# Performance work log

Hardware: AMD Instinct MI355X
Metric: run time of the kernel (lower is better)

Reference implementation:

```python
import jax, jax.numpy as jnp
import numpy as np

U, I, D, L, NNZ, B = 100000, 50000, 64, 3, 3200000, 4096
N = U + I
MOMENTUM = 0.05

def setup_inputs() -> dict:
    key = jax.random.key(0)
    ks = jax.random.split(key, 10)
    return {
        'user_emb': jax.random.normal(ks[0], (U, D), jnp.float32) * 0.02,
        'item_emb': jax.random.normal(ks[1], (I, D), jnp.float32) * 0.02,
        'W': jax.random.normal(ks[2], (D, D), jnp.float32) * (1.0 / np.sqrt(D)),
        'b': jnp.zeros((D,), jnp.float32),
        'adj_rows': jax.random.randint(ks[3], (NNZ,), 0, N, jnp.int32),
        'adj_cols': jax.random.randint(ks[4], (NNZ,), 0, N, jnp.int32),
        'adj_vals': jax.random.uniform(ks[5], (NNZ,), jnp.float32) * 0.05,
        'users': jax.random.randint(ks[6], (B,), 0, U, jnp.int32),
        'items': jax.random.randint(ks[7], (B,), 0, I, jnp.int32),
        'u_his': jax.random.normal(ks[8], (U, D), jnp.float32),
        'i_his': jax.random.normal(ks[9], (I, D), jnp.float32),
    }

def _spmm(rows, cols, vals, x):
    # y = A @ x for sparse COO A: gather source rows, scale, scatter-add to dest rows
    return jax.ops.segment_sum(vals[:, None] * x[cols], rows, num_segments=N)

def reference(user_emb, item_emb, W, b, adj_rows, adj_cols, adj_vals, users, items, u_his, i_his):
    ego = jnp.concatenate([user_emb, item_emb], axis=0)  # [N, D]
    acc = ego
    cur = ego
    for _ in range(L):
        cur = _spmm(adj_rows, adj_cols, adj_vals, cur)
        acc = acc + cur
    all_emb = acc / (L + 1)           # mean over stacked layers
    u_all = all_emb[:U]
    i_all = all_emb[U:]
    u_online = u_all[users]           # [B, D]
    i_online = i_all[items]
    m = MOMENTUM
    u_target = jax.lax.stop_gradient(u_his[users] * m + u_online * (1.0 - m))
    i_target = jax.lax.stop_gradient(i_his[items] * m + i_online * (1.0 - m))
    p_u = u_online @ W.T + b
    p_i = i_online @ W.T + b
    return (p_u, u_target, p_i, i_target)
```

## Files before the change

### kernel.cpp

```cpp
#include <hip/hip_runtime.h>
#include <hip/hip_bf16.h>

#define U_CNT   100000
#define I_CNT   50000
#define D_DIM   64
#define N_NODES 150000
#define NNZ_E   3200000
#define B_SZ    4096

#define NSUB 1172
#define CAP2 4096
#define TILE_E 8192
#define N_TILES ((NNZ_E + TILE_E - 1) / TILE_E)

#define CONV_THREADS (N_NODES * 16)
#define CONV_PER_BLK (512 * 4)
#define CONV_BLOCKS ((CONV_THREADS + CONV_PER_BLK - 1) / CONV_PER_BLK)

typedef unsigned int uint;
typedef unsigned short ushort_t;
typedef _Float16 half_t;
typedef half_t half2_t __attribute__((ext_vector_type(2)));

union h2u_t { uint u; half2_t h; };
__device__ __forceinline__ half2_t u2h2(uint u) { h2u_t c; c.u = u; return c.h; }
__device__ __forceinline__ uint h22u(half2_t h) { h2u_t c; c.h = h; return c.u; }
__device__ __forceinline__ half2_t h2shfl_xor(half2_t v, int m) {
    h2u_t c; c.h = v; c.u = (uint)__shfl_xor((int)c.u, m, 64); return c.h;
}
__device__ __forceinline__ float h2lo(uint u) { return (float)u2h2(u)[0]; }
__device__ __forceinline__ float h2hi(uint u) { return (float)u2h2(u)[1]; }

__global__ __launch_bounds__(256) void init_cursors_kernel(int* __restrict__ subcursor) {
    int i = blockIdx.x * 256 + threadIdx.x;
    if (i < NSUB) subcursor[i] = i * CAP2;
}

__global__ __launch_bounds__(512) void scatter_kernel(const int* __restrict__ rows,
                                                      const int* __restrict__ cols,
                                                      const float* __restrict__ vals,
                                                      int* __restrict__ subcursor,
                                                      int2* __restrict__ meta,
                                                      const float4* __restrict__ ue4,
                                                      const float4* __restrict__ ie4,
                                                      uint2* __restrict__ e2) {
    int tid = threadIdx.x;

    if (blockIdx.x >= N_TILES) {
        int g0 = (blockIdx.x - N_TILES) * CONV_PER_BLK + tid;
        #pragma unroll
        for (int k = 0; k < 4; ++k) {
            int g = g0 + k * 512;
            if (g < CONV_THREADS) {
                float4 f = (g < U_CNT * 16) ? ue4[g] : ie4[g - U_CNT * 16];
                half2_t a = { (half_t)f.x, (half_t)f.y };
                half2_t b = { (half_t)f.z, (half_t)f.w };
                uint2 o; o.x = h22u(a); o.y = h22u(b);
                e2[g] = o;
            }
        }
        return;
    }

    __shared__ int lcnt[NSUB];
    __shared__ int gbase[NSUB];

    for (int i = tid; i < NSUB; i += 512) lcnt[i] = 0;
    __syncthreads();

    int base = blockIdx.x * TILE_E;
    int nk = NNZ_E - base - tid;
    nk = (nk <= 0) ? 0 : (nk + 511) >> 9;

    int pk[16]; float vv[16]; int sb[16]; int rk[16];
    #pragma unroll
    for (int k = 0; k < 16; ++k) {
        if (k < nk) {
            int j = base + tid + (k << 9);
            int r = rows[j];
            int c = cols[j];
            vv[k] = vals[j];
            sb[k] = r >> 7;
            pk[k] = ((r & 127) << 18) | c;
            rk[k] = atomicAdd(&lcnt[sb[k]], 1);
        }
    }
    __syncthreads();

    for (int i = tid; i < NSUB; i += 512) {
        int c = lcnt[i];
        gbase[i] = (c > 0) ? atomicAdd(&subcursor[i], c) : 0;
    }
    __syncthreads();

    #pragma unroll
    for (int k = 0; k < 16; ++k) {
        if (k < nk) {
            int pos = gbase[sb[k]] + rk[k];
            if (pos < (sb[k] + 1) * CAP2)
                meta[pos] = make_int2(pk[k], __float_as_int(vv[k]));
        }
    }
}

__global__ __launch_bounds__(256) void row_sort_kernel(const int* __restrict__ subcursor,
                                                       int2* __restrict__ meta,
                                                       int* __restrict__ rstart,
                                                       int* __restrict__ rend) {
    __shared__ int2 stage[CAP2];
    __shared__ int rcnt[128];
    __shared__ int scan[128];
    __shared__ int cur[128];
    int g = blockIdx.x;
    int base = g * CAP2;
    int cnt = subcursor[g] - base;
    if (cnt > CAP2) cnt = CAP2;
    int tid = threadIdx.x;
    int r0 = g << 7;

    if (tid < 128) rcnt[tid] = 0;
    __syncthreads();

    for (int i = tid; i < cnt; i += 256) {
        int2 e = meta[base + i];
        stage[i] = e;
        atomicAdd(&rcnt[((uint)e.x >> 18) & 127], 1);
    }
    __syncthreads();

    if (tid < 128) scan[tid] = rcnt[tid];
    __syncthreads();
    for (int off = 1; off < 128; off <<= 1) {
        int t = (tid < 128 && tid >= off) ? scan[tid - off] : 0;
        __syncthreads();
        if (tid < 128) scan[tid] += t;
        __syncthreads();
    }
    if (tid < 128) {
        int excl = scan[tid] - rcnt[tid];
        cur[tid] = excl;
        int r = r0 + tid;
        if (r < N_NODES) {
            rstart[r] = base + excl;
            rend[r]   = base + scan[tid];
        }
    }
    __syncthreads();

    for (int i = tid; i < cnt; i += 256) {
        int2 e = stage[i];
        int rl = ((uint)e.x >> 18) & 127;
        int pos = atomicAdd(&cur[rl], 1);
        float v = __int_as_float(e.y);
        half2_t hv = { (half_t)v, (half_t)v };
        meta[base + pos] = make_int2(e.x & 0x3FFFF, (int)h22u(hv));
    }
}

__global__ __launch_bounds__(256) void spmm_fp16_kernel(const int* __restrict__ rstart,
                                                        const int* __restrict__ rend,
                                                        const int2* __restrict__ csr,
                                                        const ushort_t* __restrict__ x,
                                                        ushort_t* __restrict__ out) {
    int wid  = (blockIdx.x * blockDim.x + threadIdx.x) >> 6;
    int lane = threadIdx.x & 63;
    int sub  = lane >> 3;
    int l8   = lane & 7;
    if (wid >= N_NODES) return;
    int s = rstart[wid], e = rend[wid];
    const uint4* x4 = (const uint4*)x;

    int last = e - 1; if (last < s) last = s;
    auto ld = [&](int jj) -> int2 {
        int2 c = csr[jj < e ? jj : last];
        if (jj >= e) c.y = 0;
        return c;
    };

    half2_t a0 = { (half_t)0, (half_t)0 };
    half2_t a1 = a0, a2 = a0, a3 = a0;

    int j = s + sub;
    int2 c0 = ld(j);
    int2 c1 = ld(j + 8);
    int2 c2 = ld(j + 16);
    int2 c3 = ld(j + 24);
    for (; j < e; j += 32) {
        uint4 x0 = x4[(size_t)(c0.x & 0x3FFFF) * 8 + l8];
        uint4 x1 = x4[(size_t)(c1.x & 0x3FFFF) * 8 + l8];
        uint4 x2 = x4[(size_t)(c2.x & 0x3FFFF) * 8 + l8];
        uint4 x3 = x4[(size_t)(c3.x & 0x3FFFF) * 8 + l8];
        int jn = j + 32;
        int2 n0 = ld(jn);
        int2 n1 = ld(jn + 8);
        int2 n2 = ld(jn + 16);
        int2 n3 = ld(jn + 24);
        half2_t v0 = u2h2((uint)c0.y);
        a0 += u2h2(x0.x) * v0; a1 += u2h2(x0.y) * v0;
        a2 += u2h2(x0.z) * v0; a3 += u2h2(x0.w) * v0;
        half2_t v1 = u2h2((uint)c1.y);
        a0 += u2h2(x1.x) * v1; a1 += u2h2(x1.y) * v1;
        a2 += u2h2(x1.z) * v1; a3 += u2h2(x1.w) * v1;
        half2_t v2 = u2h2((uint)c2.y);
        a0 += u2h2(x2.x) * v2; a1 += u2h2(x2.y) * v2;
        a2 += u2h2(x2.z) * v2; a3 += u2h2(x2.w) * v2;
        half2_t v3 = u2h2((uint)c3.y);
        a0 += u2h2(x3.x) * v3; a1 += u2h2(x3.y) * v3;
        a2 += u2h2(x3.z) * v3; a3 += u2h2(x3.w) * v3;
        c0 = n0; c1 = n1; c2 = n2; c3 = n3;
    }
    a0 += h2shfl_xor(a0, 8);  a1 += h2shfl_xor(a1, 8);
    a2 += h2shfl_xor(a2, 8);  a3 += h2shfl_xor(a3, 8);
    a0 += h2shfl_xor(a0, 16); a1 += h2shfl_xor(a1, 16);
    a2 += h2shfl_xor(a2, 16); a3 += h2shfl_xor(a3, 16);
    a0 += h2shfl_xor(a0, 32); a1 += h2shfl_xor(a1, 32);
    a2 += h2shfl_xor(a2, 32); a3 += h2shfl_xor(a3, 32);

    if (sub == 0) {
        uint4 r;
        r.x = h22u(a0); r.y = h22u(a1); r.z = h22u(a2); r.w = h22u(a3);
        ((uint4*)out)[(size_t)wid * 8 + l8] = r;
    }
}

__global__ __launch_bounds__(256) void epilogue_kernel(const int* __restrict__ users,
                                                       const int* __restrict__ items,
                                                       const int* __restrict__ rstart,
                                                       const int* __restrict__ rend,
                                                       const int2* __restrict__ csr,
                                                       const ushort_t* __restrict__ ebuf,
                                                       const ushort_t* __restrict__ buf1,
                                                       const ushort_t* __restrict__ buf2,
                                                       const float* __restrict__ u_his,
                                                       const float* __restrict__ i_his,
                                                       const float* __restrict__ W,
                                                       const float* __restrict__ bvec,
                                                       float* __restrict__ out) {
    __shared__ float Wt[D_DIM * 65];
    __shared__ float bsh[D_DIM];
    __shared__ float on_s[4][D_DIM];
    for (int t = threadIdx.x; t < D_DIM * D_DIM; t += blockDim.x) {
        int j = t >> 6, k = t & 63;
        Wt[k * 65 + j] = W[t];
    }
    if (threadIdx.x < D_DIM) bsh[threadIdx.x] = bvec[threadIdx.x];

    int wv   = threadIdx.x >> 6;
    int wid  = blockIdx.x * 4 + wv;
    int lane = threadIdx.x & 63;
    int sub  = lane >> 4;
    int l16  = lane & 15;

    bool is_user = (wid < B_SZ);
    int  samp = is_user ? wid : wid - B_SZ;
    int  idx  = is_user ? users[samp] : items[samp];
    int  row  = is_user ? idx : (U_CNT + idx);

    const float* his = is_user ? u_his : i_his;
    float hisv = his[(size_t)idx * D_DIM + lane];
    uint2 eg = make_uint2(0, 0), b1v = eg, b2v = eg;
    if (sub == 0) {
        eg  = ((const uint2*)ebuf)[(size_t)row * 16 + l16];
        b1v = ((const uint2*)buf1)[(size_t)row * 16 + l16];
        b2v = ((const uint2*)buf2)[(size_t)row * 16 + l16];
    }

    int s = rstart[row], e = rend[row];
    int last = e - 1; if (last < s) last = s;
    auto ld = [&](int jj) -> int2 {
        int2 c = csr[jj < e ? jj : last];
        if (jj >= e) c.y = 0;
        return c;
    };
    half2_t c0 = { (half_t)0, (half_t)0 };
    half2_t c1 = c0;
    int j = s + sub;
    int2 e0 = ld(j);
    int2 e1 = ld(j + 4);
    int2 e2 = ld(j + 8);
    int2 e3 = ld(j + 12);
    for (; j < e; j += 16) {
        uint2 x0 = ((const uint2*)buf2)[(size_t)(e0.x & 0x3FFFF) * 16 + l16];
        uint2 x1 = ((const uint2*)buf2)[(size_t)(e1.x & 0x3FFFF) * 16 + l16];
        uint2 x2 = ((const uint2*)buf2)[(size_t)(e2.x & 0x3FFFF) * 16 + l16];
        uint2 x3 = ((const uint2*)buf2)[(size_t)(e3.x & 0x3FFFF) * 16 + l16];
        int jn = j + 16;
        int2 n0 = ld(jn);
        int2 n1 = ld(jn + 4);
        int2 n2 = ld(jn + 8);
        int2 n3 = ld(jn + 12);
        half2_t v0 = u2h2((uint)e0.y);
        c0 += u2h2(x0.x) * v0; c1 += u2h2(x0.y) * v0;
        half2_t v1 = u2h2((uint)e1.y);
        c0 += u2h2(x1.x) * v1; c1 += u2h2(x1.y) * v1;
        half2_t v2 = u2h2((uint)e2.y);
        c0 += u2h2(x2.x) * v2; c1 += u2h2(x2.y) * v2;
        half2_t v3 = u2h2((uint)e3.y);
        c0 += u2h2(x3.x) * v3; c1 += u2h2(x3.y) * v3;
        e0 = n0; e1 = n1; e2 = n2; e3 = n3;
    }
    c0 += h2shfl_xor(c0, 16); c1 += h2shfl_xor(c1, 16);
    c0 += h2shfl_xor(c0, 32); c1 += h2shfl_xor(c1, 32);

    if (sub == 0) {
        on_s[wv][l16 * 4 + 0] = (h2lo(eg.x) + h2lo(b1v.x) + h2lo(b2v.x) + (float)c0[0]) * 0.25f;
        on_s[wv][l16 * 4 + 1] = (h2hi(eg.x) + h2hi(b1v.x) + h2hi(b2v.x) + (float)c0[1]) * 0.25f;
        on_s[wv][l16 * 4 + 2] = (h2lo(eg.y) + h2lo(b1v.y) + h2lo(b2v.y) + (float)c1[0]) * 0.25f;
        on_s[wv][l16 * 4 + 3] = (h2hi(eg.y) + h2hi(b1v.y) + h2hi(b2v.y) + (float)c1[1]) * 0.25f;
    }
    __syncthreads();

    float online = on_s[wv][lane];
    float target = 0.05f * hisv + 0.95f * online;

    float p = bsh[lane];
    #pragma unroll
    for (int k = 0; k < D_DIM; ++k) {
        float ok = __shfl(online, k, 64);
        p = fmaf(ok, Wt[k * 65 + lane], p);
    }

    size_t base = is_user ? 0 : (size_t)2 * B_SZ * D_DIM;
    out[base + (size_t)samp * D_DIM + lane] = p;
    out[base + (size_t)B_SZ * D_DIM + (size_t)samp * D_DIM + lane] = target;
}


extern "C" void kernel_launch(void* const* d_in, const int* in_sizes, int n_in,
                              void* d_out, int out_size, void* d_ws, size_t ws_size,
                              hipStream_t stream) {
    const float* user_emb = (const float*)d_in[0];
    const float* item_emb = (const float*)d_in[1];
    const float* W        = (const float*)d_in[2];
    const float* bvec     = (const float*)d_in[3];
    const int*   adj_rows = (const int*)d_in[4];
    const int*   adj_cols = (const int*)d_in[5];
    const float* adj_vals = (const float*)d_in[6];
    const int*   users    = (const int*)d_in[7];
    const int*   items    = (const int*)d_in[8];
    const float* u_his    = (const float*)d_in[9];
    const float* i_his    = (const float*)d_in[10];
    float* out = (float*)d_out;

    char* ws = (char*)d_ws;
    size_t o = 0;
    ushort_t* ebuf  = (ushort_t*)(ws + o); o += (size_t)N_NODES * D_DIM * 2;
    ushort_t* buf1  = (ushort_t*)(ws + o); o += (size_t)N_NODES * D_DIM * 2;
    ushort_t* buf2  = (ushort_t*)(ws + o); o += (size_t)N_NODES * D_DIM * 2;
    int2*  meta     = (int2*)(ws + o);     o += (size_t)NSUB * CAP2 * 8;
    int*   rstart   = (int*)(ws + o);      o += (size_t)N_NODES * 4;
    int*   rend     = (int*)(ws + o);      o += (size_t)N_NODES * 4;
    int*   subcursor= (int*)(ws + o);      o += (size_t)NSUB * 4;
    (void)ws_size; (void)o; (void)in_sizes; (void)n_in; (void)out_size;

    init_cursors_kernel<<<(NSUB + 255) / 256, 256, 0, stream>>>(subcursor);
    scatter_kernel<<<N_TILES + CONV_BLOCKS, 512, 0, stream>>>(
        adj_rows, adj_cols, adj_vals, subcursor, meta,
        (const float4*)user_emb, (const float4*)item_emb, (uint2*)ebuf);
    row_sort_kernel<<<NSUB, 256, 0, stream>>>(subcursor, meta, rstart, rend);

    int spmm_blocks = (N_NODES + 3) / 4;
    spmm_fp16_kernel<<<spmm_blocks, 256, 0, stream>>>(rstart, rend, meta, ebuf, buf1);
    spmm_fp16_kernel<<<spmm_blocks, 256, 0, stream>>>(rstart, rend, meta, buf1, buf2);

    epilogue_kernel<<<(2 * B_SZ) / 4, 256, 0, stream>>>(users, items, rstart, rend, meta,
                                                        ebuf, buf1, buf2,
                                                        u_his, i_his, W, bvec, out);
}
```

Baseline: 335.0 us.

## Use larger two-pass scatter tiles and a wavefront-shuffle row scan

The COO scatter kernel now runs 256-thread blocks over 16K-edge tiles in two passes. The first pass only counts rows per sub-bucket, and the second re-reads rows, cols and vals and places each edge. This halves the number of global cursor atomics and per-block LDS initialisations, and frees the registers that held 16 staged edges. The cost is reading the row indices twice. The row_sort prefix sum over 128 rows is replaced by a single-wavefront shuffle scan over pairs, which removes the shared scan array and many barriers.

```diff
diff --git a/kernel.cpp b/kernel.cpp
--- a/kernel.cpp
+++ b/kernel.cpp
@@ -10,11 +10,11 @@
 
 #define NSUB 1172
 #define CAP2 4096
-#define TILE_E 8192
+#define TILE_E 16384
 #define N_TILES ((NNZ_E + TILE_E - 1) / TILE_E)
 
 #define CONV_THREADS (N_NODES * 16)
-#define CONV_PER_BLK (512 * 4)
+#define CONV_PER_BLK (256 * 4)
 #define CONV_BLOCKS ((CONV_THREADS + CONV_PER_BLK - 1) / CONV_PER_BLK)
 
 typedef unsigned int uint;
@@ -36,7 +36,7 @@
     if (i < NSUB) subcursor[i] = i * CAP2;
 }
 
-__global__ __launch_bounds__(512) void scatter_kernel(const int* __restrict__ rows,
+__global__ __launch_bounds__(256) void scatter_kernel(const int* __restrict__ rows,
                                                       const int* __restrict__ cols,
                                                       const float* __restrict__ vals,
                                                       int* __restrict__ subcursor,
@@ -50,7 +50,7 @@
         int g0 = (blockIdx.x - N_TILES) * CONV_PER_BLK + tid;
         #pragma unroll
         for (int k = 0; k < 4; ++k) {
-            int g = g0 + k * 512;
+            int g = g0 + k * 256;
             if (g < CONV_THREADS) {
                 float4 f = (g < U_CNT * 16) ? ue4[g] : ie4[g - U_CNT * 16];
                 half2_t a = { (half_t)f.x, (half_t)f.y };
@@ -65,40 +65,42 @@
     __shared__ int lcnt[NSUB];
     __shared__ int gbase[NSUB];
 
-    for (int i = tid; i < NSUB; i += 512) lcnt[i] = 0;
+    for (int i = tid; i < NSUB; i += 256) lcnt[i] = 0;
     __syncthreads();
 
     int base = blockIdx.x * TILE_E;
-    int nk = NNZ_E - base - tid;
-    nk = (nk <= 0) ? 0 : (nk + 511) >> 9;
-
-    int pk[16]; float vv[16]; int sb[16]; int rk[16];
-    #pragma unroll
-    for (int k = 0; k < 16; ++k) {
-        if (k < nk) {
-            int j = base + tid + (k << 9);
-            int r = rows[j];
-            int c = cols[j];
-            vv[k] = vals[j];
-            sb[k] = r >> 7;
-            pk[k] = ((r & 127) << 18) | c;
-            rk[k] = atomicAdd(&lcnt[sb[k]], 1);
+    int end = base + TILE_E; if (end > NNZ_E) end = NNZ_E;
+
+    for (int j0 = base; j0 < end; j0 += 4096) {
+        #pragma unroll
+        for (int k = 0; k < 16; ++k) {
+            int j = j0 + tid + (k << 8);
+            if (j < end) atomicAdd(&lcnt[rows[j] >> 7], 1);
         }
     }
     __syncthreads();
 
-    for (int i = tid; i < NSUB; i += 512) {
+    for (int i = tid; i < NSUB; i += 256) {
         int c = lcnt[i];
         gbase[i] = (c > 0) ? atomicAdd(&subcursor[i], c) : 0;
-    }
-    __syncthreads();
-
-    #pragma unroll
-    for (int k = 0; k < 16; ++k) {
-        if (k < nk) {
-            int pos = gbase[sb[k]] + rk[k];
-            if (pos < (sb[k] + 1) * CAP2)
-                meta[pos] = make_int2(pk[k], __float_as_int(vv[k]));
+        lcnt[i] = 0;
+    }
+    __syncthreads();
+
+    for (int j0 = base; j0 < end; j0 += 4096) {
+        #pragma unroll
+        for (int k = 0; k < 16; ++k) {
+            int j = j0 + tid + (k << 8);
+            if (j < end) {
+                int r = rows[j];
+                int c = cols[j];
+                float v = vals[j];
+                int sb = r >> 7;
+                int rk = atomicAdd(&lcnt[sb], 1);
+                int pos = gbase[sb] + rk;
+                if (pos < (sb + 1) * CAP2)
+                    meta[pos] = make_int2(((r & 127) << 18) | c, __float_as_int(v));
+            }
         }
     }
 }
@@ -109,7 +111,6 @@
                                                        int* __restrict__ rend) {
     __shared__ int2 stage[CAP2];
     __shared__ int rcnt[128];
-    __shared__ int scan[128];
     __shared__ int cur[128];
     int g = blockIdx.x;
     int base = g * CAP2;
@@ -128,22 +129,20 @@
     }
     __syncthreads();
 
-    if (tid < 128) scan[tid] = rcnt[tid];
-    __syncthreads();
-    for (int off = 1; off < 128; off <<= 1) {
-        int t = (tid < 128 && tid >= off) ? scan[tid - off] : 0;
-        __syncthreads();
-        if (tid < 128) scan[tid] += t;
-        __syncthreads();
-    }
-    if (tid < 128) {
-        int excl = scan[tid] - rcnt[tid];
-        cur[tid] = excl;
-        int r = r0 + tid;
-        if (r < N_NODES) {
-            rstart[r] = base + excl;
-            rend[r]   = base + scan[tid];
+    if (tid < 64) {
+        int c0 = rcnt[2 * tid], c1 = rcnt[2 * tid + 1];
+        int s2 = c0 + c1, incl = s2;
+        #pragma unroll
+        for (int off = 1; off < 64; off <<= 1) {
+            int t = __shfl_up(incl, off, 64);
+            if (tid >= off) incl += t;
         }
+        int s0 = incl - s2, s1 = incl - c1;
+        cur[2 * tid] = s0;
+        cur[2 * tid + 1] = s1;
+        int r = r0 + 2 * tid;
+        if (r < N_NODES)     { rstart[r]     = base + s0; rend[r]     = base + s0 + c0; }
+        if (r + 1 < N_NODES) { rstart[r + 1] = base + s1; rend[r + 1] = base + incl;    }
     }
     __syncthreads();
 
@@ -354,7 +353,7 @@
     (void)ws_size; (void)o; (void)in_sizes; (void)n_in; (void)out_size;
 
     init_cursors_kernel<<<(NSUB + 255) / 256, 256, 0, stream>>>(subcursor);
-    scatter_kernel<<<N_TILES + CONV_BLOCKS, 512, 0, stream>>>(
+    scatter_kernel<<<N_TILES + CONV_BLOCKS, 256, 0, stream>>>(
         adj_rows, adj_cols, adj_vals, subcursor, meta,
         (const float4*)user_emb, (const float4*)item_emb, (uint2*)ebuf);
     row_sort_kernel<<<NSUB, 256, 0, stream>>>(subcursor, meta, rstart, rend);
```

After: 401.7 us. 19.9% more time.

## Fuse row sort, two SpMM layers and epilogue into one cooperative persistent kernel

Applied to the files above, without the earlier changes.

Replaces the row-sort, two SpMM launches and the epilogue with a single cooperative kernel that uses grid-wide syncs between phases. The row sort now writes into a separate meta2 buffer and uses a wave-shuffle scan instead of a shared-memory scan with many barriers. The cursor init kernel becomes a memset, with the base offset added in scatter. This removes launch gaps and tail effects, at the cost of grid.sync overhead and persistent-loop occupancy limits (launch bounds of 6 blocks per CU, grid capped at 2048).

```diff
diff --git a/kernel.cpp b/kernel.cpp
--- a/kernel.cpp
+++ b/kernel.cpp
@@ -1,5 +1,8 @@
 #include <hip/hip_runtime.h>
 #include <hip/hip_bf16.h>
+#include <hip/hip_cooperative_groups.h>
+
+namespace cg = cooperative_groups;
 
 #define U_CNT   100000
 #define I_CNT   50000
@@ -17,6 +20,8 @@
 #define CONV_PER_BLK (512 * 4)
 #define CONV_BLOCKS ((CONV_THREADS + CONV_PER_BLK - 1) / CONV_PER_BLK)
 
+#define NB_EPI ((2 * B_SZ) / 4)
+
 typedef unsigned int uint;
 typedef unsigned short ushort_t;
 typedef _Float16 half_t;
@@ -30,11 +35,6 @@
 }
 __device__ __forceinline__ float h2lo(uint u) { return (float)u2h2(u)[0]; }
 __device__ __forceinline__ float h2hi(uint u) { return (float)u2h2(u)[1]; }
-
-__global__ __launch_bounds__(256) void init_cursors_kernel(int* __restrict__ subcursor) {
-    int i = blockIdx.x * 256 + threadIdx.x;
-    if (i < NSUB) subcursor[i] = i * CAP2;
-}
 
 __global__ __launch_bounds__(512) void scatter_kernel(const int* __restrict__ rows,
                                                       const int* __restrict__ cols,
@@ -89,7 +89,8 @@
 
     for (int i = tid; i < NSUB; i += 512) {
         int c = lcnt[i];
-        gbase[i] = (c > 0) ? atomicAdd(&subcursor[i], c) : 0;
+        int off = (c > 0) ? atomicAdd(&subcursor[i], c) : 0;
+        gbase[i] = i * CAP2 + off;
     }
     __syncthreads();
 
@@ -103,226 +104,234 @@
     }
 }
 
-__global__ __launch_bounds__(256) void row_sort_kernel(const int* __restrict__ subcursor,
-                                                       int2* __restrict__ meta,
+__device__ __forceinline__ void spmm_phase(int wbase, int nwaves, int lane,
+                                           const int* __restrict__ rstart,
+                                           const int* __restrict__ rend,
+                                           const int2* __restrict__ csr,
+                                           const ushort_t* __restrict__ x,
+                                           ushort_t* __restrict__ out) {
+    int sub = lane >> 3;
+    int l8  = lane & 7;
+    const uint4* x4 = (const uint4*)x;
+
+    for (int wid = wbase; wid < N_NODES; wid += nwaves) {
+        int s = rstart[wid], e = rend[wid];
+        int last = e - 1; if (last < s) last = s;
+        auto ld = [&](int jj) -> int2 {
+            int2 c = csr[jj < e ? jj : last];
+            if (jj >= e) c.y = 0;
+            return c;
+        };
+
+        half2_t a0 = { (half_t)0, (half_t)0 };
+        half2_t a1 = a0, a2 = a0, a3 = a0;
+
+        int j = s + sub;
+        int2 c0 = ld(j);
+        int2 c1 = ld(j + 8);
+        int2 c2 = ld(j + 16);
+        int2 c3 = ld(j + 24);
+        for (; j < e; j += 32) {
+            uint4 x0 = x4[(size_t)(c0.x & 0x3FFFF) * 8 + l8];
+            uint4 x1 = x4[(size_t)(c1.x & 0x3FFFF) * 8 + l8];
+            uint4 x2 = x4[(size_t)(c2.x & 0x3FFFF) * 8 + l8];
+            uint4 x3 = x4[(size_t)(c3.x & 0x3FFFF) * 8 + l8];
+            int jn = j + 32;
+            int2 n0 = ld(jn);
+            int2 n1 = ld(jn + 8);
+            int2 n2 = ld(jn + 16);
+            int2 n3 = ld(jn + 24);
+            half2_t v0 = u2h2((uint)c0.y);
+            a0 += u2h2(x0.x) * v0; a1 += u2h2(x0.y) * v0;
+            a2 += u2h2(x0.z) * v0; a3 += u2h2(x0.w) * v0;
+            half2_t v1 = u2h2((uint)c1.y);
+            a0 += u2h2(x1.x) * v1; a1 += u2h2(x1.y) * v1;
+            a2 += u2h2(x1.z) * v1; a3 += u2h2(x1.w) * v1;
+            half2_t v2 = u2h2((uint)c2.y);
+            a0 += u2h2(x2.x) * v2; a1 += u2h2(x2.y) * v2;
+            a2 += u2h2(x2.z) * v2; a3 += u2h2(x2.w) * v2;
+            half2_t v3 = u2h2((uint)c3.y);
+            a0 += u2h2(x3.x) * v3; a1 += u2h2(x3.y) * v3;
+            a2 += u2h2(x3.z) * v3; a3 += u2h2(x3.w) * v3;
+            c0 = n0; c1 = n1; c2 = n2; c3 = n3;
+        }
+        a0 += h2shfl_xor(a0, 8);  a1 += h2shfl_xor(a1, 8);
+        a2 += h2shfl_xor(a2, 8);  a3 += h2shfl_xor(a3, 8);
+        a0 += h2shfl_xor(a0, 16); a1 += h2shfl_xor(a1, 16);
+        a2 += h2shfl_xor(a2, 16); a3 += h2shfl_xor(a3, 16);
+        a0 += h2shfl_xor(a0, 32); a1 += h2shfl_xor(a1, 32);
+        a2 += h2shfl_xor(a2, 32); a3 += h2shfl_xor(a3, 32);
+
+        if (sub == 0) {
+            uint4 r;
+            r.x = h22u(a0); r.y = h22u(a1); r.z = h22u(a2); r.w = h22u(a3);
+            ((uint4*)out)[(size_t)wid * 8 + l8] = r;
+        }
+    }
+}
+
+__global__ __launch_bounds__(256, 6) void fused_kernel(const int* __restrict__ subcursor,
+                                                       const int2* __restrict__ meta,
+                                                       int2* __restrict__ meta2,
                                                        int* __restrict__ rstart,
-                                                       int* __restrict__ rend) {
-    __shared__ int2 stage[CAP2];
-    __shared__ int rcnt[128];
-    __shared__ int scan[128];
-    __shared__ int cur[128];
-    int g = blockIdx.x;
-    int base = g * CAP2;
-    int cnt = subcursor[g] - base;
-    if (cnt > CAP2) cnt = CAP2;
-    int tid = threadIdx.x;
-    int r0 = g << 7;
-
-    if (tid < 128) rcnt[tid] = 0;
-    __syncthreads();
-
-    for (int i = tid; i < cnt; i += 256) {
-        int2 e = meta[base + i];
-        stage[i] = e;
-        atomicAdd(&rcnt[((uint)e.x >> 18) & 127], 1);
-    }
-    __syncthreads();
-
-    if (tid < 128) scan[tid] = rcnt[tid];
-    __syncthreads();
-    for (int off = 1; off < 128; off <<= 1) {
-        int t = (tid < 128 && tid >= off) ? scan[tid - off] : 0;
-        __syncthreads();
-        if (tid < 128) scan[tid] += t;
-        __syncthreads();
-    }
-    if (tid < 128) {
-        int excl = scan[tid] - rcnt[tid];
-        cur[tid] = excl;
-        int r = r0 + tid;
-        if (r < N_NODES) {
-            rstart[r] = base + excl;
-            rend[r]   = base + scan[tid];
-        }
-    }
-    __syncthreads();
-
-    for (int i = tid; i < cnt; i += 256) {
-        int2 e = stage[i];
-        int rl = ((uint)e.x >> 18) & 127;
-        int pos = atomicAdd(&cur[rl], 1);
-        float v = __int_as_float(e.y);
-        half2_t hv = { (half_t)v, (half_t)v };
-        meta[base + pos] = make_int2(e.x & 0x3FFFF, (int)h22u(hv));
-    }
-}
-
-__global__ __launch_bounds__(256) void spmm_fp16_kernel(const int* __restrict__ rstart,
-                                                        const int* __restrict__ rend,
-                                                        const int2* __restrict__ csr,
-                                                        const ushort_t* __restrict__ x,
-                                                        ushort_t* __restrict__ out) {
-    int wid  = (blockIdx.x * blockDim.x + threadIdx.x) >> 6;
-    int lane = threadIdx.x & 63;
-    int sub  = lane >> 3;
-    int l8   = lane & 7;
-    if (wid >= N_NODES) return;
-    int s = rstart[wid], e = rend[wid];
-    const uint4* x4 = (const uint4*)x;
-
-    int last = e - 1; if (last < s) last = s;
-    auto ld = [&](int jj) -> int2 {
-        int2 c = csr[jj < e ? jj : last];
-        if (jj >= e) c.y = 0;
-        return c;
-    };
-
-    half2_t a0 = { (half_t)0, (half_t)0 };
-    half2_t a1 = a0, a2 = a0, a3 = a0;
-
-    int j = s + sub;
-    int2 c0 = ld(j);
-    int2 c1 = ld(j + 8);
-    int2 c2 = ld(j + 16);
-    int2 c3 = ld(j + 24);
-    for (; j < e; j += 32) {
-        uint4 x0 = x4[(size_t)(c0.x & 0x3FFFF) * 8 + l8];
-        uint4 x1 = x4[(size_t)(c1.x & 0x3FFFF) * 8 + l8];
-        uint4 x2 = x4[(size_t)(c2.x & 0x3FFFF) * 8 + l8];
-        uint4 x3 = x4[(size_t)(c3.x & 0x3FFFF) * 8 + l8];
-        int jn = j + 32;
-        int2 n0 = ld(jn);
-        int2 n1 = ld(jn + 8);
-        int2 n2 = ld(jn + 16);
-        int2 n3 = ld(jn + 24);
-        half2_t v0 = u2h2((uint)c0.y);
-        a0 += u2h2(x0.x) * v0; a1 += u2h2(x0.y) * v0;
-        a2 += u2h2(x0.z) * v0; a3 += u2h2(x0.w) * v0;
-        half2_t v1 = u2h2((uint)c1.y);
-        a0 += u2h2(x1.x) * v1; a1 += u2h2(x1.y) * v1;
-        a2 += u2h2(x1.z) * v1; a3 += u2h2(x1.w) * v1;
-        half2_t v2 = u2h2((uint)c2.y);
-        a0 += u2h2(x2.x) * v2; a1 += u2h2(x2.y) * v2;
-        a2 += u2h2(x2.z) * v2; a3 += u2h2(x2.w) * v2;
-        half2_t v3 = u2h2((uint)c3.y);
-        a0 += u2h2(x3.x) * v3; a1 += u2h2(x3.y) * v3;
-        a2 += u2h2(x3.z) * v3; a3 += u2h2(x3.w) * v3;
-        c0 = n0; c1 = n1; c2 = n2; c3 = n3;
-    }
-    a0 += h2shfl_xor(a0, 8);  a1 += h2shfl_xor(a1, 8);
-    a2 += h2shfl_xor(a2, 8);  a3 += h2shfl_xor(a3, 8);
-    a0 += h2shfl_xor(a0, 16); a1 += h2shfl_xor(a1, 16);
-    a2 += h2shfl_xor(a2, 16); a3 += h2shfl_xor(a3, 16);
-    a0 += h2shfl_xor(a0, 32); a1 += h2shfl_xor(a1, 32);
-    a2 += h2shfl_xor(a2, 32); a3 += h2shfl_xor(a3, 32);
-
-    if (sub == 0) {
-        uint4 r;
-        r.x = h22u(a0); r.y = h22u(a1); r.z = h22u(a2); r.w = h22u(a3);
-        ((uint4*)out)[(size_t)wid * 8 + l8] = r;
-    }
-}
-
-__global__ __launch_bounds__(256) void epilogue_kernel(const int* __restrict__ users,
+                                                       int* __restrict__ rend,
+                                                       const ushort_t* __restrict__ ebuf,
+                                                       ushort_t* __restrict__ buf1,
+                                                       ushort_t* __restrict__ buf2,
+                                                       const int* __restrict__ users,
                                                        const int* __restrict__ items,
-                                                       const int* __restrict__ rstart,
-                                                       const int* __restrict__ rend,
-                                                       const int2* __restrict__ csr,
-                                                       const ushort_t* __restrict__ ebuf,
-                                                       const ushort_t* __restrict__ buf1,
-                                                       const ushort_t* __restrict__ buf2,
                                                        const float* __restrict__ u_his,
                                                        const float* __restrict__ i_his,
                                                        const float* __restrict__ W,
                                                        const float* __restrict__ bvec,
                                                        float* __restrict__ out) {
+    cg::grid_group grid = cg::this_grid();
+    int tid = threadIdx.x;
+
+    __shared__ int rcnt[128];
+    __shared__ int cur[128];
     __shared__ float Wt[D_DIM * 65];
     __shared__ float bsh[D_DIM];
     __shared__ float on_s[4][D_DIM];
-    for (int t = threadIdx.x; t < D_DIM * D_DIM; t += blockDim.x) {
+
+    for (int g = blockIdx.x; g < NSUB; g += gridDim.x) {
+        int base = g * CAP2;
+        int cnt = subcursor[g];
+        if (cnt > CAP2) cnt = CAP2;
+        int r0 = g << 7;
+
+        if (tid < 128) rcnt[tid] = 0;
+        __syncthreads();
+
+        for (int i = tid; i < cnt; i += 256)
+            atomicAdd(&rcnt[((uint)meta[base + i].x >> 18) & 127], 1);
+        __syncthreads();
+
+        if (tid < 64) {
+            int c0 = rcnt[2 * tid], c1 = rcnt[2 * tid + 1];
+            int s2 = c0 + c1, incl = s2;
+            #pragma unroll
+            for (int off = 1; off < 64; off <<= 1) {
+                int t = __shfl_up(incl, off, 64);
+                if (tid >= off) incl += t;
+            }
+            int s0 = incl - s2, s1 = incl - c1;
+            cur[2 * tid] = s0;
+            cur[2 * tid + 1] = s1;
+            int r = r0 + 2 * tid;
+            if (r < N_NODES)     { rstart[r]     = base + s0; rend[r]     = base + s0 + c0; }
+            if (r + 1 < N_NODES) { rstart[r + 1] = base + s1; rend[r + 1] = base + incl;    }
+        }
+        __syncthreads();
+
+        for (int i = tid; i < cnt; i += 256) {
+            int2 e = meta[base + i];
+            int rl = ((uint)e.x >> 18) & 127;
+            int pos = atomicAdd(&cur[rl], 1);
+            float v = __int_as_float(e.y);
+            half2_t hv = { (half_t)v, (half_t)v };
+            meta2[base + pos] = make_int2(e.x & 0x3FFFF, (int)h22u(hv));
+        }
+        __syncthreads();
+    }
+    grid.sync();
+
+    int lane   = tid & 63;
+    int nwaves = (gridDim.x * 256) >> 6;
+    int wbase  = (blockIdx.x * 256 + tid) >> 6;
+
+    spmm_phase(wbase, nwaves, lane, rstart, rend, meta2, ebuf, buf1);
+    grid.sync();
+    spmm_phase(wbase, nwaves, lane, rstart, rend, meta2, buf1, buf2);
+    grid.sync();
+
+    for (int t = tid; t < D_DIM * D_DIM; t += 256) {
         int j = t >> 6, k = t & 63;
         Wt[k * 65 + j] = W[t];
     }
-    if (threadIdx.x < D_DIM) bsh[threadIdx.x] = bvec[threadIdx.x];
-
-    int wv   = threadIdx.x >> 6;
-    int wid  = blockIdx.x * 4 + wv;
-    int lane = threadIdx.x & 63;
-    int sub  = lane >> 4;
-    int l16  = lane & 15;
-
-    bool is_user = (wid < B_SZ);
-    int  samp = is_user ? wid : wid - B_SZ;
-    int  idx  = is_user ? users[samp] : items[samp];
-    int  row  = is_user ? idx : (U_CNT + idx);
-
-    const float* his = is_user ? u_his : i_his;
-    float hisv = his[(size_t)idx * D_DIM + lane];
-    uint2 eg = make_uint2(0, 0), b1v = eg, b2v = eg;
-    if (sub == 0) {
-        eg  = ((const uint2*)ebuf)[(size_t)row * 16 + l16];
-        b1v = ((const uint2*)buf1)[(size_t)row * 16 + l16];
-        b2v = ((const uint2*)buf2)[(size_t)row * 16 + l16];
-    }
-
-    int s = rstart[row], e = rend[row];
-    int last = e - 1; if (last < s) last = s;
-    auto ld = [&](int jj) -> int2 {
-        int2 c = csr[jj < e ? jj : last];
-        if (jj >= e) c.y = 0;
-        return c;
-    };
-    half2_t c0 = { (half_t)0, (half_t)0 };
-    half2_t c1 = c0;
-    int j = s + sub;
-    int2 e0 = ld(j);
-    int2 e1 = ld(j + 4);
-    int2 e2 = ld(j + 8);
-    int2 e3 = ld(j + 12);
-    for (; j < e; j += 16) {
-        uint2 x0 = ((const uint2*)buf2)[(size_t)(e0.x & 0x3FFFF) * 16 + l16];
-        uint2 x1 = ((const uint2*)buf2)[(size_t)(e1.x & 0x3FFFF) * 16 + l16];
-        uint2 x2 = ((const uint2*)buf2)[(size_t)(e2.x & 0x3FFFF) * 16 + l16];
-        uint2 x3 = ((const uint2*)buf2)[(size_t)(e3.x & 0x3FFFF) * 16 + l16];
-        int jn = j + 16;
-        int2 n0 = ld(jn);
-        int2 n1 = ld(jn + 4);
-        int2 n2 = ld(jn + 8);
-        int2 n3 = ld(jn + 12);
-        half2_t v0 = u2h2((uint)e0.y);
-        c0 += u2h2(x0.x) * v0; c1 += u2h2(x0.y) * v0;
-        half2_t v1 = u2h2((uint)e1.y);
-        c0 += u2h2(x1.x) * v1; c1 += u2h2(x1.y) * v1;
-        half2_t v2 = u2h2((uint)e2.y);
-        c0 += u2h2(x2.x) * v2; c1 += u2h2(x2.y) * v2;
-        half2_t v3 = u2h2((uint)e3.y);
-        c0 += u2h2(x3.x) * v3; c1 += u2h2(x3.y) * v3;
-        e0 = n0; e1 = n1; e2 = n2; e3 = n3;
-    }
-    c0 += h2shfl_xor(c0, 16); c1 += h2shfl_xor(c1, 16);
-    c0 += h2shfl_xor(c0, 32); c1 += h2shfl_xor(c1, 32);
-
-    if (sub == 0) {
-        on_s[wv][l16 * 4 + 0] = (h2lo(eg.x) + h2lo(b1v.x) + h2lo(b2v.x) + (float)c0[0]) * 0.25f;
-        on_s[wv][l16 * 4 + 1] = (h2hi(eg.x) + h2hi(b1v.x) + h2hi(b2v.x) + (float)c0[1]) * 0.25f;
-        on_s[wv][l16 * 4 + 2] = (h2lo(eg.y) + h2lo(b1v.y) + h2lo(b2v.y) + (float)c1[0]) * 0.25f;
-        on_s[wv][l16 * 4 + 3] = (h2hi(eg.y) + h2hi(b1v.y) + h2hi(b2v.y) + (float)c1[1]) * 0.25f;
-    }
+    if (tid < D_DIM) bsh[tid] = bvec[tid];
     __syncthreads();
 
-    float online = on_s[wv][lane];
-    float target = 0.05f * hisv + 0.95f * online;
-
-    float p = bsh[lane];
-    #pragma unroll
-    for (int k = 0; k < D_DIM; ++k) {
-        float ok = __shfl(online, k, 64);
-        p = fmaf(ok, Wt[k * 65 + lane], p);
-    }
-
-    size_t base = is_user ? 0 : (size_t)2 * B_SZ * D_DIM;
-    out[base + (size_t)samp * D_DIM + lane] = p;
-    out[base + (size_t)B_SZ * D_DIM + (size_t)samp * D_DIM + lane] = target;
+    int wv  = tid >> 6;
+    int sub = lane >> 4;
+    int l16 = lane & 15;
+
+    for (int b = blockIdx.x; b < NB_EPI; b += gridDim.x) {
+        int wid = b * 4 + wv;
+        bool is_user = (wid < B_SZ);
+        int  samp = is_user ? wid : wid - B_SZ;
+        int  idx  = is_user ? users[samp] : items[samp];
+        int  row  = is_user ? idx : (U_CNT + idx);
+
+        const float* his = is_user ? u_his : i_his;
+        float hisv = his[(size_t)idx * D_DIM + lane];
+        uint2 eg = make_uint2(0, 0), b1v = eg, b2v = eg;
+        if (sub == 0) {
+            eg  = ((const uint2*)ebuf)[(size_t)row * 16 + l16];
+            b1v = ((const uint2*)buf1)[(size_t)row * 16 + l16];
+            b2v = ((const uint2*)buf2)[(size_t)row * 16 + l16];
+        }
+
+        int s = rstart[row], e = rend[row];
+        int last = e - 1; if (last < s) last = s;
+        auto ld = [&](int jj) -> int2 {
+            int2 c = meta2[jj < e ? jj : last];
+            if (jj >= e) c.y = 0;
+            return c;
+        };
+        half2_t c0 = { (half_t)0, (half_t)0 };
+        half2_t c1 = c0;
+        int j = s + sub;
+        int2 e0 = ld(j);
+        int2 e1 = ld(j + 4);
+        int2 e2 = ld(j + 8);
+        int2 e3 = ld(j + 12);
+        for (; j < e; j += 16) {
+            uint2 x0 = ((const uint2*)buf2)[(size_t)(e0.x & 0x3FFFF) * 16 + l16];
+            uint2 x1 = ((const uint2*)buf2)[(size_t)(e1.x & 0x3FFFF) * 16 + l16];
+            uint2 x2 = ((const uint2*)buf2)[(size_t)(e2.x & 0x3FFFF) * 16 + l16];
+            uint2 x3 = ((const uint2*)buf2)[(size_t)(e3.x & 0x3FFFF) * 16 + l16];
+            int jn = j + 16;
+            int2 n0 = ld(jn);
+            int2 n1 = ld(jn + 4);
+            int2 n2 = ld(jn + 8);
+            int2 n3 = ld(jn + 12);
+            half2_t v0 = u2h2((uint)e0.y);
+            c0 += u2h2(x0.x) * v0; c1 += u2h2(x0.y) * v0;
+            half2_t v1 = u2h2((uint)e1.y);
+            c0 += u2h2(x1.x) * v1; c1 += u2h2(x1.y) * v1;
+            half2_t v2 = u2h2((uint)e2.y);
+            c0 += u2h2(x2.x) * v2; c1 += u2h2(x2.y) * v2;
+            half2_t v3 = u2h2((uint)e3.y);
+            c0 += u2h2(x3.x) * v3; c1 += u2h2(x3.y) * v3;
+            e0 = n0; e1 = n1; e2 = n2; e3 = n3;
+        }
+        c0 += h2shfl_xor(c0, 16); c1 += h2shfl_xor(c1, 16);
+        c0 += h2shfl_xor(c0, 32); c1 += h2shfl_xor(c1, 32);
+
+        if (sub == 0) {
+            on_s[wv][l16 * 4 + 0] = (h2lo(eg.x) + h2lo(b1v.x) + h2lo(b2v.x) + (float)c0[0]) * 0.25f;
+            on_s[wv][l16 * 4 + 1] = (h2hi(eg.x) + h2hi(b1v.x) + h2hi(b2v.x) + (float)c0[1]) * 0.25f;
+            on_s[wv][l16 * 4 + 2] = (h2lo(eg.y) + h2lo(b1v.y) + h2lo(b2v.y) + (float)c1[0]) * 0.25f;
+            on_s[wv][l16 * 4 + 3] = (h2hi(eg.y) + h2hi(b1v.y) + h2hi(b2v.y) + (float)c1[1]) * 0.25f;
+        }
+        __syncthreads();
+
+        float online = on_s[wv][lane];
+        float target = 0.05f * hisv + 0.95f * online;
+
+        float p = bsh[lane];
+        #pragma unroll
+        for (int k = 0; k < D_DIM; ++k) {
+            float ok = __shfl(online, k, 64);
+            p = fmaf(ok, Wt[k * 65 + lane], p);
+        }
+
+        size_t obase = is_user ? 0 : (size_t)2 * B_SZ * D_DIM;
+        out[obase + (size_t)samp * D_DIM + lane] = p;
+        out[obase + (size_t)B_SZ * D_DIM + (size_t)samp * D_DIM + lane] = target;
+        __syncthreads();
+    }
 }
 
 
@@ -348,22 +357,32 @@
     ushort_t* buf1  = (ushort_t*)(ws + o); o += (size_t)N_NODES * D_DIM * 2;
     ushort_t* buf2  = (ushort_t*)(ws + o); o += (size_t)N_NODES * D_DIM * 2;
     int2*  meta     = (int2*)(ws + o);     o += (size_t)NSUB * CAP2 * 8;
+    int2*  meta2    = (int2*)(ws + o);     o += (size_t)NSUB * CAP2 * 8;
     int*   rstart   = (int*)(ws + o);      o += (size_t)N_NODES * 4;
     int*   rend     = (int*)(ws + o);      o += (size_t)N_NODES * 4;
     int*   subcursor= (int*)(ws + o);      o += (size_t)NSUB * 4;
     (void)ws_size; (void)o; (void)in_sizes; (void)n_in; (void)out_size;
 
-    init_cursors_kernel<<<(NSUB + 255) / 256, 256, 0, stream>>>(subcursor);
+    hipMemsetAsync(subcursor, 0, (size_t)NSUB * 4, stream);
+
     scatter_kernel<<<N_TILES + CONV_BLOCKS, 512, 0, stream>>>(
         adj_rows, adj_cols, adj_vals, subcursor, meta,
         (const float4*)user_emb, (const float4*)item_emb, (uint2*)ebuf);
-    row_sort_kernel<<<NSUB, 256, 0, stream>>>(subcursor, meta, rstart, rend);
-
-    int spmm_blocks = (N_NODES + 3) / 4;
-    spmm_fp16_kernel<<<spmm_blocks, 256, 0, stream>>>(rstart, rend, meta, ebuf, buf1);
-    spmm_fp16_kernel<<<spmm_blocks, 256, 0, stream>>>(rstart, rend, meta, buf1, buf2);
-
-    epilogue_kernel<<<(2 * B_SZ) / 4, 256, 0, stream>>>(users, items, rstart, rend, meta,
-                                                        ebuf, buf1, buf2,
-                                                        u_his, i_his, W, bvec, out);
-}
+
+    int nb = 0;
+    hipOccupancyMaxActiveBlocksPerMultiprocessor(&nb, (const void*)fused_kernel, 256, 0);
+    if (nb < 1) nb = 1;
+    long grid_l = (long)nb * 256;
+    if (grid_l > 2048) grid_l = 2048;
+    dim3 grid((uint)grid_l), block(256);
+
+    void* kargs[] = {
+        (void*)&subcursor, (void*)&meta, (void*)&meta2,
+        (void*)&rstart, (void*)&rend,
+        (void*)&ebuf, (void*)&buf1, (void*)&buf2,
+        (void*)&users, (void*)&items,
+        (void*)&u_his, (void*)&i_his,
+        (void*)&W, (void*)&bvec, (void*)&out
+    };
+    hipLaunchCooperativeKernel((void*)fused_kernel, grid, block, kargs, 0, stream);
+}
```

After: 717.3 us. 2.14x slower.

## Fuse row sort with first SpMM layer reading edges from shared memory

Applied to the files above, without the earlier changes.

The per-subgroup row sort now also computes the first SpMM layer for its 128 rows, reading the sorted edges straight from LDS instead of reloading them from global memory in a separate kernel. The sort uses register-held per-thread ranks and a wave-shuffle scan in place of a second LDS atomic pass and a barrier-heavy scan. The cursor init kernel becomes a memset, with base offsets added in the scatter. In exchange, only 1172 blocks of 512 threads run the first layer, each wave handling 16 rows one after another, so there is less parallelism and load imbalance can hurt.

```diff
diff --git a/kernel.cpp b/kernel.cpp
--- a/kernel.cpp
+++ b/kernel.cpp
@@ -30,11 +30,6 @@
 }
 __device__ __forceinline__ float h2lo(uint u) { return (float)u2h2(u)[0]; }
 __device__ __forceinline__ float h2hi(uint u) { return (float)u2h2(u)[1]; }
-
-__global__ __launch_bounds__(256) void init_cursors_kernel(int* __restrict__ subcursor) {
-    int i = blockIdx.x * 256 + threadIdx.x;
-    if (i < NSUB) subcursor[i] = i * CAP2;
-}
 
 __global__ __launch_bounds__(512) void scatter_kernel(const int* __restrict__ rows,
                                                       const int* __restrict__ cols,
@@ -89,7 +84,8 @@
 
     for (int i = tid; i < NSUB; i += 512) {
         int c = lcnt[i];
-        gbase[i] = (c > 0) ? atomicAdd(&subcursor[i], c) : 0;
+        int off = (c > 0) ? atomicAdd(&subcursor[i], c) : 0;
+        gbase[i] = i * CAP2 + off;
     }
     __syncthreads();
 
@@ -103,17 +99,19 @@
     }
 }
 
-__global__ __launch_bounds__(256) void row_sort_kernel(const int* __restrict__ subcursor,
-                                                       int2* __restrict__ meta,
-                                                       int* __restrict__ rstart,
-                                                       int* __restrict__ rend) {
+__global__ __launch_bounds__(512) void sort_spmm_kernel(const int* __restrict__ subcursor,
+                                                        int2* __restrict__ meta,
+                                                        int* __restrict__ rstart,
+                                                        int* __restrict__ rend,
+                                                        const ushort_t* __restrict__ x,
+                                                        ushort_t* __restrict__ out) {
     __shared__ int2 stage[CAP2];
     __shared__ int rcnt[128];
-    __shared__ int scan[128];
-    __shared__ int cur[128];
+    __shared__ int rs[128];
+    __shared__ int re_[128];
     int g = blockIdx.x;
     int base = g * CAP2;
-    int cnt = subcursor[g] - base;
+    int cnt = subcursor[g];
     if (cnt > CAP2) cnt = CAP2;
     int tid = threadIdx.x;
     int r0 = g << 7;
@@ -121,39 +119,111 @@
     if (tid < 128) rcnt[tid] = 0;
     __syncthreads();
 
-    for (int i = tid; i < cnt; i += 256) {
-        int2 e = meta[base + i];
-        stage[i] = e;
-        atomicAdd(&rcnt[((uint)e.x >> 18) & 127], 1);
-    }
-    __syncthreads();
-
-    if (tid < 128) scan[tid] = rcnt[tid];
-    __syncthreads();
-    for (int off = 1; off < 128; off <<= 1) {
-        int t = (tid < 128 && tid >= off) ? scan[tid - off] : 0;
-        __syncthreads();
-        if (tid < 128) scan[tid] += t;
-        __syncthreads();
-    }
-    if (tid < 128) {
-        int excl = scan[tid] - rcnt[tid];
-        cur[tid] = excl;
-        int r = r0 + tid;
-        if (r < N_NODES) {
-            rstart[r] = base + excl;
-            rend[r]   = base + scan[tid];
-        }
-    }
-    __syncthreads();
-
-    for (int i = tid; i < cnt; i += 256) {
-        int2 e = stage[i];
-        int rl = ((uint)e.x >> 18) & 127;
-        int pos = atomicAdd(&cur[rl], 1);
-        float v = __int_as_float(e.y);
-        half2_t hv = { (half_t)v, (half_t)v };
-        meta[base + pos] = make_int2(e.x & 0x3FFFF, (int)h22u(hv));
+    int2 ek[8]; int rk[8];
+    int nk = cnt - tid;
+    nk = (nk <= 0) ? 0 : (nk + 511) >> 9;
+    #pragma unroll
+    for (int k = 0; k < 8; ++k) {
+        if (k < nk) {
+            ek[k] = meta[base + tid + (k << 9)];
+            rk[k] = atomicAdd(&rcnt[((uint)ek[k].x >> 18) & 127], 1);
+        }
+    }
+    __syncthreads();
+
+    if (tid < 64) {
+        int c0 = rcnt[2 * tid], c1 = rcnt[2 * tid + 1];
+        int s2 = c0 + c1, incl = s2;
+        #pragma unroll
+        for (int off = 1; off < 64; off <<= 1) {
+            int t = __shfl_up(incl, off, 64);
+            if (tid >= off) incl += t;
+        }
+        int s0 = incl - s2, s1 = incl - c1;
+        rs[2 * tid] = s0;      re_[2 * tid] = s0 + c0;
+        rs[2 * tid + 1] = s1;  re_[2 * tid + 1] = incl;
+        int r = r0 + 2 * tid;
+        if (r < N_NODES)     { rstart[r]     = base + s0; rend[r]     = base + s0 + c0; }
+        if (r + 1 < N_NODES) { rstart[r + 1] = base + s1; rend[r + 1] = base + incl;    }
+    }
+    __syncthreads();
+
+    #pragma unroll
+    for (int k = 0; k < 8; ++k) {
+        if (k < nk) {
+            int rl = ((uint)ek[k].x >> 18) & 127;
+            int pos = rs[rl] + rk[k];
+            float v = __int_as_float(ek[k].y);
+            half2_t hv = { (half_t)v, (half_t)v };
+            int2 f = make_int2(ek[k].x & 0x3FFFF, (int)h22u(hv));
+            stage[pos] = f;
+            meta[base + pos] = f;
+        }
+    }
+    __syncthreads();
+
+    int wv   = tid >> 6;
+    int lane = tid & 63;
+    int sub  = lane >> 3;
+    int l8   = lane & 7;
+    const uint4* x4 = (const uint4*)x;
+
+    for (int rr = 0; rr < 16; ++rr) {
+        int rl = (wv << 4) + rr;
+        int s = rs[rl], e = re_[rl];
+        half2_t a0 = { (half_t)0, (half_t)0 };
+        half2_t a1 = a0, a2 = a0, a3 = a0;
+
+        if (e > s) {
+            int last = e - 1;
+            auto ldl = [&](int jj) -> int2 {
+                int2 c = stage[jj < e ? jj : last];
+                if (jj >= e) c.y = 0;
+                return c;
+            };
+            int j = s + sub;
+            int2 c0 = ldl(j);
+            int2 c1 = ldl(j + 8);
+            int2 c2 = ldl(j + 16);
+            int2 c3 = ldl(j + 24);
+            for (; j < e; j += 32) {
+                uint4 x0 = x4[(size_t)(c0.x & 0x3FFFF) * 8 + l8];
+                uint4 x1 = x4[(size_t)(c1.x & 0x3FFFF) * 8 + l8];
+                uint4 x2 = x4[(size_t)(c2.x & 0x3FFFF) * 8 + l8];
+                uint4 x3 = x4[(size_t)(c3.x & 0x3FFFF) * 8 + l8];
+                int jn = j + 32;
+                int2 n0 = ldl(jn);
+                int2 n1 = ldl(jn + 8);
+                int2 n2 = ldl(jn + 16);
+                int2 n3 = ldl(jn + 24);
+                half2_t v0 = u2h2((uint)c0.y);
+                a0 += u2h2(x0.x) * v0; a1 += u2h2(x0.y) * v0;
+                a2 += u2h2(x0.z) * v0; a3 += u2h2(x0.w) * v0;
+                half2_t v1 = u2h2((uint)c1.y);
+                a0 += u2h2(x1.x) * v1; a1 += u2h2(x1.y) * v1;
+                a2 += u2h2(x1.z) * v1; a3 += u2h2(x1.w) * v1;
+                half2_t v2 = u2h2((uint)c2.y);
+                a0 += u2h2(x2.x) * v2; a1 += u2h2(x2.y) * v2;
+                a2 += u2h2(x2.z) * v2; a3 += u2h2(x2.w) * v2;
+                half2_t v3 = u2h2((uint)c3.y);
+                a0 += u2h2(x3.x) * v3; a1 += u2h2(x3.y) * v3;
+                a2 += u2h2(x3.z) * v3; a3 += u2h2(x3.w) * v3;
+                c0 = n0; c1 = n1; c2 = n2; c3 = n3;
+            }
+        }
+        a0 += h2shfl_xor(a0, 8);  a1 += h2shfl_xor(a1, 8);
+        a2 += h2shfl_xor(a2, 8);  a3 += h2shfl_xor(a3, 8);
+        a0 += h2shfl_xor(a0, 16); a1 += h2shfl_xor(a1, 16);
+        a2 += h2shfl_xor(a2, 16); a3 += h2shfl_xor(a3, 16);
+        a0 += h2shfl_xor(a0, 32); a1 += h2shfl_xor(a1, 32);
+        a2 += h2shfl_xor(a2, 32); a3 += h2shfl_xor(a3, 32);
+
+        int wid = r0 + rl;
+        if (sub == 0 && wid < N_NODES) {
+            uint4 r;
+            r.x = h22u(a0); r.y = h22u(a1); r.z = h22u(a2); r.w = h22u(a3);
+            ((uint4*)out)[(size_t)wid * 8 + l8] = r;
+        }
     }
 }
 
@@ -353,14 +423,16 @@
     int*   subcursor= (int*)(ws + o);      o += (size_t)NSUB * 4;
     (void)ws_size; (void)o; (void)in_sizes; (void)n_in; (void)out_size;
 
-    init_cursors_kernel<<<(NSUB + 255) / 256, 256, 0, stream>>>(subcursor);
+    hipMemsetAsync(subcursor, 0, (size_t)NSUB * 4, stream);
+
     scatter_kernel<<<N_TILES + CONV_BLOCKS, 512, 0, stream>>>(
         adj_rows, adj_cols, adj_vals, subcursor, meta,
         (const float4*)user_emb, (const float4*)item_emb, (uint2*)ebuf);
-    row_sort_kernel<<<NSUB, 256, 0, stream>>>(subcursor, meta, rstart, rend);
+
+    sort_spmm_kernel<<<NSUB, 512, 0, stream>>>(subcursor, meta, rstart, rend,
+                                               ebuf, buf1);
 
     int spmm_blocks = (N_NODES + 3) / 4;
-    spmm_fp16_kernel<<<spmm_blocks, 256, 0, stream>>>(rstart, rend, meta, ebuf, buf1);
     spmm_fp16_kernel<<<spmm_blocks, 256, 0, stream>>>(rstart, rend, meta, buf1, buf2);
 
     epilogue_kernel<<<(2 * B_SZ) / 4, 256, 0, stream>>>(users, items, rstart, rend, meta,
```

Result: no change. 329.0 us (-1.8%).
